# Performance work log

Measured on AMD Instinct MI355X. Metric: run time of the kernel, lower is better.

The kernel has to match this reference:

```python
import jax, jax.numpy as jnp
import numpy as np

M, K, N = 8192, 4096, 4096
ALPHA, BETA = 0.002, 0.0005


def setup_inputs() -> dict:
    key = jax.random.key(0)
    kx, kw, kb = jax.random.split(key, 3)
    # int8-range quantized activations and weights (stored as int32 for portability)
    x = jax.random.randint(kx, (M, K), -127, 127, dtype=jnp.int32)
    weight = jax.random.randint(kw, (N, K), -127, 127, dtype=jnp.int32)  # (out, in)
    bias = jax.random.randint(kb, (1, N), -(2**20), 2**20, dtype=jnp.int32)
    alpha = jnp.float32(ALPHA)
    beta = jnp.float32(BETA)
    return {"x": x, "weight": weight, "bias": bias, "alpha": alpha, "beta": beta}


def reference(x, weight, bias, alpha, beta):
    # int8 GEMM with int32 accumulation: acc[m, n] = sum_k x[m, k] * W[n, k]
    acc = jnp.matmul(x, weight.T, preferred_element_type=jnp.int32)  # [M, N] int32
    # CUTLASS-style epilogue: D = round(alpha * acc + beta * bias) -> int32
    y = alpha * acc.astype(jnp.float32) + beta * bias.astype(jnp.float32)
    return jnp.round(y).astype(jnp.int32)
```

## Files before the change

kernel.cpp:

```cpp
#include <hip/hip_runtime.h>
#include <hip/hip_bf16.h>
#include <stdint.h>

#define M_DIM 8192
#define N_DIM 4096
#define K_DIM 4096

#define BM 256
#define BN 256
#define BK 64
#define NT (K_DIM / BK)
#define DEPTH 4

typedef int v4i __attribute__((ext_vector_type(4)));

#define AS1C(p) ((const __attribute__((address_space(1))) void*)(p))
#define AS3(p)  ((__attribute__((address_space(3))) void*)(p))

__device__ __forceinline__ int pack4(int a, int b, int c, int d) {
  return (a & 0xff) | ((b & 0xff) << 8) | ((c & 0xff) << 16) | (d << 24);
}

__global__ void pack_both_kernel(const int* __restrict__ x, const int* __restrict__ w,
                                 char* __restrict__ A8, char* __restrict__ B8,
                                 int nA, int nTot) {
  int idx = blockIdx.x * blockDim.x + threadIdx.x;
  int stride = gridDim.x * blockDim.x;
  for (int i = idx; i < nTot; i += stride) {
    const int4* pin;
    int4* pout;
    if (i < nA) {
      pin  = (const int4*)x + 4 * (size_t)i;
      pout = (int4*)A8 + i;
    } else {
      int j = i - nA;
      pin  = (const int4*)w + 4 * (size_t)j;
      pout = (int4*)B8 + j;
    }
    int4 v0 = pin[0];
    int4 v1 = pin[1];
    int4 v2 = pin[2];
    int4 v3 = pin[3];
    int4 o;
    o.x = pack4(v0.x, v0.y, v0.z, v0.w);
    o.y = pack4(v1.x, v1.y, v1.z, v1.w);
    o.z = pack4(v2.x, v2.y, v2.z, v2.w);
    o.w = pack4(v3.x, v3.y, v3.z, v3.w);
    *pout = o;
  }
}

__global__ __launch_bounds__(512, 2) void gemm_i8_kernel(
    const char* __restrict__ A8, const char* __restrict__ B8,
    const int* __restrict__ bias, const float* __restrict__ alpha_p,
    const float* __restrict__ beta_p, int* __restrict__ out) {
  __shared__ alignas(16) char lds[DEPTH][BM * BK + BN * BK];

  const int tid  = threadIdx.x;
  const int lane = tid & 63;
  const int wave = tid >> 6;

  const int orig = blockIdx.x;
  const int swz  = (orig & 7) * (512 / 8) + (orig >> 3);
  const int bm   = (swz >> 4) * BM;
  const int bn   = (swz & 15) * BN;

  int aoff[2], boff[2], ldsoff[2];
#pragma unroll
  for (int i = 0; i < 2; ++i) {
    int linear = i * 8192 + tid * 16;
    int row = linear >> 6;
    int p   = (linear >> 4) & 3;
    int g   = p ^ ((row >> 1) & 3);
    ldsoff[i] = i * 8192 + wave * 1024;
    aoff[i] = (bm + row) * K_DIM + g * 16;
    boff[i] = (bn + row) * K_DIM + g * 16;
  }

#define STAGE_A(t)                                                                  \
  do {                                                                              \
    const char* ab_ = A8 + (size_t)(t) * BK;                                        \
    char* base_ = &lds[(t) & (DEPTH - 1)][0];                                       \
    _Pragma("unroll") for (int i_ = 0; i_ < 2; ++i_)                                \
      __builtin_amdgcn_global_load_lds(AS1C(ab_ + aoff[i_]),                        \
                                       AS3(base_ + ldsoff[i_]), 16, 0, 0);          \
  } while (0)

#define STAGE_B(t)                                                                  \
  do {                                                                              \
    const char* bb_ = B8 + (size_t)(t) * BK;                                        \
    char* base_ = &lds[(t) & (DEPTH - 1)][0];                                       \
    _Pragma("unroll") for (int i_ = 0; i_ < 2; ++i_)                                \
      __builtin_amdgcn_global_load_lds(AS1C(bb_ + boff[i_]),                        \
                                       AS3(base_ + 16384 + ldsoff[i_]), 16, 0, 0);  \
  } while (0)

  v4i acc[8][4];
#pragma unroll
  for (int i = 0; i < 8; ++i)
#pragma unroll
    for (int j = 0; j < 4; ++j) acc[i][j] = (v4i){0, 0, 0, 0};

  const int wr = wave >> 2;
  const int wc = wave & 3;
  const int frow = lane & 15;
  const int fchunk = lane >> 4;
  const int swzoff = ((fchunk ^ ((frow >> 1) & 3)) << 4);

  v4i bf0[4], aflo0[4], bf1[4], aflo1[4], afhi[4];

#define READ0(S, t)                                                                 \
  do {                                                                              \
    const char* base_ = &lds[(t) & (DEPTH - 1)][0];                                 \
    _Pragma("unroll") for (int nj = 0; nj < 4; ++nj)                                \
      bf##S[nj] = *(const v4i*)(base_ + 16384 + (wc * 64 + nj * 16 + frow) * 64 +   \
                                swzoff);                                            \
    _Pragma("unroll") for (int mi = 0; mi < 4; ++mi)                                \
      aflo##S[mi] = *(const v4i*)(base_ + (wr * 128 + mi * 16 + frow) * 64 +        \
                                  swzoff);                                          \
  } while (0)

#define READ1(t)                                                                    \
  do {                                                                              \
    const char* base_ = &lds[(t) & (DEPTH - 1)][0];                                 \
    _Pragma("unroll") for (int mi = 0; mi < 4; ++mi)                                \
      afhi[mi] = *(const v4i*)(base_ + (wr * 128 + (mi + 4) * 16 + frow) * 64 +     \
                               swzoff);                                             \
  } while (0)

#define MFMA_LO(S)                                                                  \
  do {                                                                              \
    __builtin_amdgcn_s_setprio(1);                                                  \
    _Pragma("unroll") for (int mi = 0; mi < 4; ++mi)                                \
      _Pragma("unroll") for (int nj = 0; nj < 4; ++nj)                              \
        acc[mi][nj] = __builtin_amdgcn_mfma_i32_16x16x64_i8(aflo##S[mi], bf##S[nj], \
                                                            acc[mi][nj], 0, 0, 0); \
    __builtin_amdgcn_s_setprio(0);                                                  \
  } while (0)

#define MFMA_HI(S)                                                                  \
  do {                                                                              \
    __builtin_amdgcn_s_setprio(1);                                                  \
    _Pragma("unroll") for (int mi = 0; mi < 4; ++mi)                                \
      _Pragma("unroll") for (int nj = 0; nj < 4; ++nj)                              \
        acc[mi + 4][nj] = __builtin_amdgcn_mfma_i32_16x16x64_i8(afhi[mi], bf##S[nj],\
                                                                acc[mi + 4][nj],   \
                                                                0, 0, 0);          \
    __builtin_amdgcn_s_setprio(0);                                                  \
  } while (0)

#define TILE(t, C, N, STG, EV)                                                      \
  do {                                                                              \
    if (STG) STAGE_A((t) + 3);                                                      \
    READ1(t);                                                                       \
    MFMA_LO(C);                                                                     \
    if (STG) STAGE_B((t) + 3);                                                      \
    if ((t) + 1 < NT) READ0(N, (t) + 1);                                            \
    MFMA_HI(C);                                                                     \
    if ((EV) == 4) asm volatile("s_waitcnt vmcnt(4)" ::: "memory");                 \
    if ((EV) == 0) asm volatile("s_waitcnt vmcnt(0)" ::: "memory");                 \
    if ((EV) >= 0) __builtin_amdgcn_s_barrier();                                    \
  } while (0)

  STAGE_A(0); STAGE_B(0);
  STAGE_A(1); STAGE_B(1);
  STAGE_A(2); STAGE_B(2);
  asm volatile("s_waitcnt vmcnt(4)" ::: "memory");
  __builtin_amdgcn_s_barrier();
  READ0(0, 0);

  for (int t = 0; t < NT - 4; t += 2) {
    TILE(t, 0, 1, true, 4);
    TILE(t + 1, 1, 0, true, 4);
  }
  TILE(NT - 4, 0, 1, true, 4);
  TILE(NT - 3, 1, 0, false, 0);
  TILE(NT - 2, 0, 1, false, -1);
  TILE(NT - 1, 1, 0, false, -1);

  const float alpha = *alpha_p;
  const float beta  = *beta_p;
  const int col0 = bn + wc * 64 + frow;
  float bb4[4];
#pragma unroll
  for (int nj = 0; nj < 4; ++nj) bb4[nj] = beta * (float)bias[col0 + nj * 16];

  const int rbase = bm + wr * 128 + (lane >> 4) * 4;
#pragma unroll
  for (int mi = 0; mi < 8; ++mi) {
#pragma unroll
    for (int r = 0; r < 4; ++r) {
      size_t rowoff = (size_t)(rbase + mi * 16 + r) * N_DIM;
#pragma unroll
      for (int nj = 0; nj < 4; ++nj) {
        out[rowoff + col0 + nj * 16] =
            (int)rintf(fmaf(alpha, (float)acc[mi][nj][r], bb4[nj]));
      }
    }
  }
#undef STAGE_A
#undef STAGE_B
#undef READ0
#undef READ1
#undef MFMA_LO
#undef MFMA_HI
#undef TILE
}

__global__ void naive_kernel(const int* __restrict__ x, const int* __restrict__ w,
                             const int* __restrict__ bias,
                             const float* __restrict__ alpha_p,
                             const float* __restrict__ beta_p,
                             int* __restrict__ out) {
  size_t idx = (size_t)blockIdx.x * 256 + threadIdx.x;
  int m = (int)(idx / N_DIM);
  int n = (int)(idx % N_DIM);
  const int4* xr = (const int4*)(x + (size_t)m * K_DIM);
  const int4* wr = (const int4*)(w + (size_t)n * K_DIM);
  int acc = 0;
  for (int k = 0; k < K_DIM / 4; ++k) {
    int4 a = xr[k];
    int4 b = wr[k];
    acc += a.x * b.x + a.y * b.y + a.z * b.z + a.w * b.w;
  }
  out[idx] = (int)rintf(fmaf(*alpha_p, (float)acc, (*beta_p) * (float)bias[n]));
}

extern "C" void kernel_launch(void* const* d_in, const int* in_sizes, int n_in,
                              void* d_out, int out_size, void* d_ws, size_t ws_size,
                              hipStream_t stream) {
  const int*   x     = (const int*)d_in[0];
  const int*   w     = (const int*)d_in[1];
  const int*   bias  = (const int*)d_in[2];
  const float* alpha = (const float*)d_in[3];
  const float* beta  = (const float*)d_in[4];
  int* out = (int*)d_out;

  const size_t a8_bytes = (size_t)M_DIM * K_DIM;
  const size_t b8_bytes = (size_t)N_DIM * K_DIM;

  if (ws_size >= a8_bytes + b8_bytes) {
    char* A8 = (char*)d_ws;
    char* B8 = A8 + a8_bytes;
    const int nA = (int)(a8_bytes / 16);
    const int nTot = (int)((a8_bytes + b8_bytes) / 16);
    pack_both_kernel<<<2048, 256, 0, stream>>>(x, w, A8, B8, nA, nTot);
    const int nblk = (M_DIM / BM) * (N_DIM / BN);
    gemm_i8_kernel<<<nblk, 512, 0, stream>>>(A8, B8, bias, alpha, beta, out);
  } else {
    naive_kernel<<<(M_DIM * (size_t)N_DIM) / 256, 256, 0, stream>>>(x, w, bias, alpha, beta, out);
  }
}
```

Baseline: 182.4 us.

## Stagger MFMA and memory-op order between wave groups for ping-pong overlap

Splits the workgroup's waves into two groups by wave index. One group keeps the original per-tile order: stage the global loads, read LDS, then run MFMAs. The other group issues its MFMAs first and does the staging and LDS reads afterwards. The aim is that while one group waits on memory the other keeps the matrix units busy, reducing contention between the groups. The cost is a duplicated main loop, which increases code size and register-allocation pressure, and the barrier count per tile stays the same.

```diff
diff --git a/kernel.cpp b/kernel.cpp
--- a/kernel.cpp
+++ b/kernel.cpp
@@ -149,7 +149,14 @@
     __builtin_amdgcn_s_setprio(0);                                                  \
   } while (0)
 
-#define TILE(t, C, N, STG, EV)                                                      \
+#define EVWAIT(EV)                                                                  \
+  do {                                                                              \
+    if ((EV) == 4) asm volatile("s_waitcnt vmcnt(4)" ::: "memory");                 \
+    if ((EV) == 0) asm volatile("s_waitcnt vmcnt(0)" ::: "memory");                 \
+    if ((EV) >= 0) __builtin_amdgcn_s_barrier();                                    \
+  } while (0)
+
+#define TILE_E(t, C, N, STG, EV)                                                    \
   do {                                                                              \
     if (STG) STAGE_A((t) + 3);                                                      \
     READ1(t);                                                                       \
@@ -157,9 +164,18 @@
     if (STG) STAGE_B((t) + 3);                                                      \
     if ((t) + 1 < NT) READ0(N, (t) + 1);                                            \
     MFMA_HI(C);                                                                     \
-    if ((EV) == 4) asm volatile("s_waitcnt vmcnt(4)" ::: "memory");                 \
-    if ((EV) == 0) asm volatile("s_waitcnt vmcnt(0)" ::: "memory");                 \
-    if ((EV) >= 0) __builtin_amdgcn_s_barrier();                                    \
+    EVWAIT(EV);                                                                     \
+  } while (0)
+
+#define TILE_O(t, C, N, STG, EV)                                                    \
+  do {                                                                              \
+    MFMA_LO(C);                                                                     \
+    if (STG) STAGE_A((t) + 3);                                                      \
+    READ1(t);                                                                       \
+    MFMA_HI(C);                                                                     \
+    if (STG) STAGE_B((t) + 3);                                                      \
+    if ((t) + 1 < NT) READ0(N, (t) + 1);                                            \
+    EVWAIT(EV);                                                                     \
   } while (0)
 
   STAGE_A(0); STAGE_B(0);
@@ -169,14 +185,25 @@
   __builtin_amdgcn_s_barrier();
   READ0(0, 0);
 
-  for (int t = 0; t < NT - 4; t += 2) {
-    TILE(t, 0, 1, true, 4);
-    TILE(t + 1, 1, 0, true, 4);
-  }
-  TILE(NT - 4, 0, 1, true, 4);
-  TILE(NT - 3, 1, 0, false, 0);
-  TILE(NT - 2, 0, 1, false, -1);
-  TILE(NT - 1, 1, 0, false, -1);
+  if ((wave & 4) == 0) {
+    for (int t = 0; t < NT - 4; t += 2) {
+      TILE_E(t, 0, 1, true, 4);
+      TILE_E(t + 1, 1, 0, true, 4);
+    }
+    TILE_E(NT - 4, 0, 1, true, 4);
+    TILE_E(NT - 3, 1, 0, false, 0);
+    TILE_E(NT - 2, 0, 1, false, -1);
+    TILE_E(NT - 1, 1, 0, false, -1);
+  } else {
+    for (int t = 0; t < NT - 4; t += 2) {
+      TILE_O(t, 0, 1, true, 4);
+      TILE_O(t + 1, 1, 0, true, 4);
+    }
+    TILE_O(NT - 4, 0, 1, true, 4);
+    TILE_O(NT - 3, 1, 0, false, 0);
+    TILE_O(NT - 2, 0, 1, false, -1);
+    TILE_O(NT - 1, 1, 0, false, -1);
+  }
 
   const float alpha = *alpha_p;
   const float beta  = *beta_p;
@@ -204,7 +231,9 @@
 #undef READ1
 #undef MFMA_LO
 #undef MFMA_HI
-#undef TILE
+#undef EVWAIT
+#undef TILE_E
+#undef TILE_O
 }
 
 __global__ void naive_kernel(const int* __restrict__ x, const int* __restrict__ w,
```

Measured after the change: 180.5 us (median of 2 runs). Within noise of the previous version (-1.1%).
